# Optimization experiments

Measured on AMD Instinct MI355X. Metric: run time of the kernel, lower is better.

## Reference

```python
import jax, jax.numpy as jnp
import numpy as np

N_FREQ = 5
K = 16  # nneigh


def _gather(points, idx):
    # points: [B,N,C], idx: [B,nQ,K] -> [B,nQ,K,C]
    return jax.vmap(lambda p, i: p[i])(points, idx)


def setup_inputs() -> dict:
    key = jax.random.key(0)
    ks = jax.random.split(key, 16)
    B, nQ, N, dim_inp, dim = 2, 8192, 4096, 128, 128
    s = dim_inp ** -0.5
    return {
        "xyz_q": jax.random.uniform(ks[0], (B, nQ, 2), jnp.float32),
        "lat_rep": jax.random.normal(ks[1], (B, dim_inp), jnp.float32),
        "xyz": jax.random.uniform(ks[2], (B, N, 3), jnp.float32),
        "points": jax.random.normal(ks[3], (B, N, dim_inp), jnp.float32),
        "w_qs": jax.random.normal(ks[4], (dim_inp, dim), jnp.float32) * s,
        "w_ks": jax.random.normal(ks[5], (dim_inp, dim), jnp.float32) * s,
        "w_vs": jax.random.normal(ks[6], (dim_inp, dim), jnp.float32) * s,
        "w_kg": jax.random.normal(ks[7], (dim_inp, dim), jnp.float32) * s,
        "w_vg": jax.random.normal(ks[8], (dim_inp, dim), jnp.float32) * s,
        "gamma_w1": jax.random.normal(ks[9], (dim, dim), jnp.float32) * (dim ** -0.5),
        "gamma_b1": jnp.zeros((dim,), jnp.float32),
        "gamma_w2": jax.random.normal(ks[10], (dim, dim), jnp.float32) * (dim ** -0.5),
        "gamma_b2": jnp.zeros((dim,), jnp.float32),
        "pe_w": jax.random.normal(ks[11], (3 * 2 * N_FREQ + 3, dim), jnp.float32) * (33 ** -0.5),
        "pe_b": jnp.zeros((dim,), jnp.float32),
    }


def reference(xyz_q, lat_rep, xyz, points, w_qs, w_ks, w_vs, w_kg, w_vg,
              gamma_w1, gamma_b1, gamma_w2, gamma_b2, pe_w, pe_b):
    b, nQ, _ = xyz_q.shape
    dim = w_qs.shape[1]
    # kNN in 2D (no_grad in original): squared distance [B,nQ,N]
    dists = jnp.sum((xyz_q[:, :, None] - xyz[:, None, :, :2]) ** 2, axis=-1)
    _, knn_idx = jax.lax.top_k(-dists, K)  # ascending distance order

    # global latent [B,dim_inp] branch
    q_attn = (lat_rep @ w_qs)[:, None, None, :]          # [B,1,1,dim]
    k_global = jnp.broadcast_to((lat_rep @ w_kg)[:, None, None, :], (b, nQ, 1, dim))
    v_global = jnp.broadcast_to((lat_rep @ w_vg)[:, None, None, :], (b, nQ, 1, dim))

    k_attn = jnp.concatenate([_gather(points @ w_ks, knn_idx), k_global], axis=2)  # [B,nQ,K+1,dim]
    v_attn = jnp.concatenate([_gather(points @ w_vs, knn_idx), v_global], axis=2)

    xyz_knn = _gather(xyz, knn_idx)                      # [B,nQ,K,3]
    pos_diff = jnp.concatenate(
        [xyz_q[:, :, None] - xyz_knn[..., :2], xyz_knn[..., -1:]], axis=-1)  # [B,nQ,K,3]
    freq_bands = jnp.linspace(1.0, 2.0 ** N_FREQ, N_FREQ)
    embeds = [pos_diff]
    for fr in freq_bands:
        embeds.append(jnp.sin(pos_diff * fr))
        embeds.append(jnp.cos(pos_diff * fr))
    pos_embed = jnp.concatenate(embeds, axis=-1)         # [B,nQ,K,33]
    pos_encode = pos_embed @ pe_w + pe_b                 # [B,nQ,K,dim]
    pos_encode = jnp.concatenate(
        [pos_encode, jnp.zeros((b, nQ, 1, dim), pos_encode.dtype)], axis=2)  # [B,nQ,K+1,dim]

    h = q_attn - k_attn + pos_encode
    h = jnp.maximum(h @ gamma_w1 + gamma_b1, 0.0) @ gamma_w2 + gamma_b2
    attn = jax.nn.softmax(h, axis=-2)                    # softmax over neighbor axis
    res = jnp.sum(attn * (v_attn + pos_encode), axis=2)  # einsum 'bmnf,bmnf->bmf'
    return res
```

## Files before the change

### kernel.cpp

```cpp
#include <hip/hip_runtime.h>
#include <cstdint>

#define DIM   128
#define KNN   16
#define NB    2
#define NQ    8192
#define NPTS  4096
#define KVROWS 16
#define GRID  32
#define NCELL (GRID*GRID)
#define CAP   384

typedef unsigned short ushort_t;
typedef short vshort8 __attribute__((ext_vector_type(8)));
typedef float vfloat4 __attribute__((ext_vector_type(4)));

__device__ __forceinline__ ushort_t bf16_rne(float f) {
    unsigned u = __float_as_uint(f);
    unsigned r = u + 0x7FFFu + ((u >> 16) & 1u);
    return (ushort_t)(r >> 16);
}
__device__ __forceinline__ int cell_of(float x) {
    int c = (int)(x * 32.0f);
    return min(max(c, 0), GRID - 1);
}
__device__ __forceinline__ float f4_at(float4 v, int i) {
    return (i == 0) ? v.x : (i == 1) ? v.y : (i == 2) ? v.z : v.w;
}

__device__ __forceinline__ void pack_body(
    const float* __restrict__ src, int K, int ncols, int NT, int KS,
    ushort_t* __restrict__ dst, int gid)
{
    int total = NT*KS*64;
    if (gid >= total) return;
    int lane = gid & 63; int c = gid >> 6;
    int s = c % KS; int n = c / KS;
    int k0 = s*32 + ((lane >> 4) << 3);
    int col = n*16 + (lane & 15);
    vshort8 v;
    #pragma unroll
    for (int i = 0; i < 8; ++i) {
        int k = k0 + i;
        float f = (k < K) ? src[k*ncols + col] : 0.f;
        v[i] = (short)bf16_rne(f);
    }
    *(vshort8*)(dst + gid*8) = v;
}

__device__ __forceinline__ void scan1024(
    const int* __restrict__ cnt, int* __restrict__ cs, int* __restrict__ cu,
    int* __restrict__ ss, int t)
{
    int v0 = cnt[t*4 + 0];
    int v1 = cnt[t*4 + 1];
    int v2 = cnt[t*4 + 2];
    int v3 = cnt[t*4 + 3];
    int p0 = v0, p1 = p0 + v1, p2 = p1 + v2, p3 = p2 + v3;
    ss[t] = p3;
    __syncthreads();
    for (int off = 1; off < 256; off <<= 1) {
        int add = (t >= off) ? ss[t - off] : 0;
        __syncthreads();
        ss[t] += add;
        __syncthreads();
    }
    int excl = ss[t] - p3;
    cs[t*4 + 0] = excl;        cu[t*4 + 0] = excl;
    cs[t*4 + 1] = excl + p0;   cu[t*4 + 1] = excl + p0;
    cs[t*4 + 2] = excl + p1;   cu[t*4 + 2] = excl + p1;
    cs[t*4 + 3] = excl + p2;   cu[t*4 + 3] = excl + p2;
    if (t == 255) cs[NCELL] = ss[255];
}

__global__ __launch_bounds__(256) void pre1_k(
    const float* __restrict__ w_ks, const float* __restrict__ g_w1,
    const float* __restrict__ pe_w, const float* __restrict__ xyz,
    const float* __restrict__ xyz_q,
    float* __restrict__ Wk1, float* __restrict__ pwc,
    int* __restrict__ cellcnt, int* __restrict__ qcnt)
{
    int t = threadIdx.x; int bx = blockIdx.x;
    if (bx < 64) {
        int row = bx*2 + (t >> 7); int f = t & 127;
        float acc = 0.f;
        for (int c = 0; c < 128; ++c) acc = fmaf(w_ks[row*128 + c], g_w1[c*128 + f], acc);
        Wk1[row*128 + f] = acc;
    } else if (bx < 128) {
        int r = bx - 64; int col = t;
        float v = 0.f;
        if (r < 33) {
            if (col < 128) {
                float a = 0.f;
                for (int c = 0; c < 128; ++c) a = fmaf(pe_w[r*128 + c], g_w1[c*128 + col], a);
                v = a;
            } else {
                v = pe_w[r*128 + (col - 128)];
            }
        }
        pwc[r*256 + col] = v;
    } else if (bx < 160) {
        int gid = (bx - 128)*256 + t;
        int b = gid >> 12; int n = gid & (NPTS - 1);
        const float* p = xyz + (b*NPTS + n)*3;
        atomicAdd(&cellcnt[b*NCELL + cell_of(p[1])*GRID + cell_of(p[0])], 1);
    } else {
        int gid = (bx - 160)*256 + t;
        int b = gid >> 13; int q = gid & (NQ - 1);
        const float* p = xyz_q + (b*NQ + q)*2;
        atomicAdd(&qcnt[b*NCELL + cell_of(p[1])*GRID + cell_of(p[0])], 1);
    }
}

__global__ __launch_bounds__(256) void pre2_k(
    const float* __restrict__ pwc, const float* __restrict__ g_w2,
    const int* __restrict__ cnt, const int* __restrict__ qcnt,
    const float* __restrict__ lat, const float* __restrict__ w_qs,
    const float* __restrict__ w_kg, const float* __restrict__ w_vg,
    const float* __restrict__ g_w1, const float* __restrict__ g_b1,
    const float* __restrict__ pe_b,
    ushort_t* __restrict__ pwf, ushort_t* __restrict__ w2f,
    int* __restrict__ cell_start, int* __restrict__ cursor,
    int* __restrict__ qstart, int* __restrict__ qcursor,
    float* __restrict__ c1_out, float* __restrict__ vg_out, float* __restrict__ h2g_out)
{
    __shared__ int ss[256];
    __shared__ float qs[NB][DIM];
    __shared__ float hgx[NB][DIM];
    __shared__ float h1gx[NB][DIM];
    int t = threadIdx.x; int bx = blockIdx.x;
    if (bx < 4) {
        pack_body(pwc, 32, 256, 16, 1, pwf, bx*256 + t);
    } else if (bx < 12) {
        pack_body(g_w2, 128, 128, 8, 4, w2f, (bx - 4)*256 + t);
    } else if (bx < 14) {
        int b = bx - 12;
        scan1024(cnt + b*NCELL, cell_start + b*(NCELL+1), cursor + b*NCELL, ss, t);
    } else if (bx < 16) {
        int b = bx - 14;
        scan1024(qcnt + b*NCELL, qstart + b*(NCELL+1), qcursor + b*NCELL, ss, t);
    } else {
        int b = t >> 7; int f = t & 127;
        float aq = 0.f, ak = 0.f, av = 0.f;
        for (int c = 0; c < DIM; ++c) {
            float l = lat[b*DIM + c];
            aq = fmaf(l, w_qs[c*DIM + f], aq);
            ak = fmaf(l, w_kg[c*DIM + f], ak);
            av = fmaf(l, w_vg[c*DIM + f], av);
        }
        vg_out[b*DIM + f] = av;
        qs[b][f] = aq + pe_b[f];
        hgx[b][f] = aq - ak;
        __syncthreads();
        float acc = g_b1[f], acch = g_b1[f];
        for (int c = 0; c < DIM; ++c) {
            float w = g_w1[c*DIM + f];
            acc  = fmaf(qs[b][c], w, acc);
            acch = fmaf(hgx[b][c], w, acch);
        }
        c1_out[b*DIM + f] = acc;
        h1gx[b][f] = fmaxf(acch, 0.f);
        __syncthreads();
        float acc2 = 0.f;
        for (int c = 0; c < DIM; ++c) acc2 = fmaf(h1gx[b][c], g_w2[c*DIM + f], acc2);
        h2g_out[b*DIM + f] = acc2;
    }
}

__global__ __launch_bounds__(256) void pre3_k(
    const float* __restrict__ xyz, const float* __restrict__ xyz_q,
    int* __restrict__ cursor, int* __restrict__ qcursor,
    float2* __restrict__ sxy, int* __restrict__ sidx,
    float2* __restrict__ qsxy, int* __restrict__ qsidx)
{
    int t = threadIdx.x; int bx = blockIdx.x;
    if (bx < 32) {
        int gid = bx*256 + t;
        int b = gid >> 12; int n = gid & (NPTS - 1);
        const float* p = xyz + (b*NPTS + n)*3;
        float x = p[0], y = p[1];
        int slot = atomicAdd(&cursor[b*NCELL + cell_of(y)*GRID + cell_of(x)], 1);
        sxy[b*NPTS + slot] = make_float2(x, y);
        sidx[b*NPTS + slot] = n;
    } else {
        int gid = (bx - 32)*256 + t;
        int b = gid >> 13; int q = gid & (NQ - 1);
        const float* p = xyz_q + (b*NQ + q)*2;
        float x = p[0], y = p[1];
        int slot = atomicAdd(&qcursor[b*NCELL + cell_of(y)*GRID + cell_of(x)], 1);
        qsxy[b*NQ + slot] = make_float2(x, y);
        qsidx[b*NQ + slot] = q;
    }
}

__global__ __launch_bounds__(256) void knnkv_k(
    const float* __restrict__ points, const float* __restrict__ Wk1,
    const float* __restrict__ w_vs, const float* __restrict__ pe_b,
    const float* __restrict__ c1_,
    const float2* __restrict__ qsxy, const float2* __restrict__ sxy,
    const int* __restrict__ sidx, const int* __restrict__ cstart,
    float* __restrict__ K1c, float* __restrict__ Vp,
    int* __restrict__ knn_out)
{
    __shared__ __align__(16) float smem[4*CAP*2];
    int t = threadIdx.x; int bx = blockIdx.x;

    if (bx < 512) {
        float* pts = smem;
        int r0 = bx * KVROWS;
        int b = r0 >> 12;
        #pragma unroll
        for (int k = 0; k < KVROWS*DIM/256; ++k) {
            int e = t + k*256;
            pts[e] = points[r0*DIM + e];
        }
        __syncthreads();
        int f = t & 127; int mat = t >> 7;
        const float* W = mat ? w_vs : Wk1;
        float* O = mat ? Vp : K1c;
        float addv = mat ? pe_b[f] : c1_[b*DIM + f];
        float sgn  = mat ? 1.f : -1.f;
        int fc = (f & 15)*8 + (f >> 4);
        float acc[KVROWS];
        #pragma unroll
        for (int r = 0; r < KVROWS; ++r) acc[r] = 0.f;
        const float4* pts4 = reinterpret_cast<const float4*>(pts);
        for (int c4 = 0; c4 < DIM/4; ++c4) {
            float w0 = W[(c4*4+0)*DIM + f];
            float w1 = W[(c4*4+1)*DIM + f];
            float w2 = W[(c4*4+2)*DIM + f];
            float w3 = W[(c4*4+3)*DIM + f];
            #pragma unroll
            for (int r = 0; r < KVROWS; ++r) {
                float4 p = pts4[r*(DIM/4) + c4];
                acc[r] = fmaf(p.x, w0, acc[r]);
                acc[r] = fmaf(p.y, w1, acc[r]);
                acc[r] = fmaf(p.z, w2, acc[r]);
                acc[r] = fmaf(p.w, w3, acc[r]);
            }
        }
        #pragma unroll
        for (int r = 0; r < KVROWS; ++r) O[(r0 + r)*DIM + fc] = fmaf(sgn, acc[r], addv);
        return;
    }

    int bxk = bx - 512;
    int wid = t >> 6, lane = t & 63;
    int b = bxk >> 11; int q = (bxk & 2047)*4 + wid;
    float* cd = smem + wid*CAP;
    int*   ci = (int*)(smem + 4*CAP) + wid*CAP;
    float2 qp = qsxy[b*NQ + q];
    float xq = qp.x, yq = qp.y;
    int cx = cell_of(xq), cy = cell_of(yq);
    const int* cs_b = cstart + b*(NCELL+1);
    const float INF = 3.4e38f;
    const float CS = 1.0f/32.0f;
    int* outp = knn_out + (b*NQ + q)*KNN;
    unsigned long long lmask = (1ull << lane) - 1ull;

    for (int R = 2; R < 9; ++R) {
        int x0 = max(cx-R, 0), x1 = min(cx+R, GRID-1);
        int y0 = max(cy-R, 0), y1 = min(cy+R, GRID-1);
        int cnt = 0;
        for (int ry = y0; ry <= y1; ++ry) {
            int s0 = cs_b[ry*GRID + x0];
            int e0 = cs_b[ry*GRID + x1 + 1];
            for (int o = s0 + lane; o < e0; o += 64) {
                float2 p = sxy[b*NPTS + o];
                float dx = __fadd_rn(xq, -p.x);
                float dy = __fadd_rn(yq, -p.y);
                float d = __fadd_rn(__fmul_rn(dx, dx), __fmul_rn(dy, dy));
                int slot = cnt + (o - s0);
                if (slot < CAP) { cd[slot] = d; ci[slot] = o; }
            }
            cnt += e0 - s0;
        }
        asm volatile("s_waitcnt lgkmcnt(0)" ::: "memory");
        __builtin_amdgcn_sched_barrier(0);

        int cc = min(cnt, CAP);
        float dr[6];
        #pragma unroll
        for (int k = 0; k < 6; ++k)
            dr[k] = (lane + k*64 < cc) ? cd[lane + k*64] : INF;

        unsigned lo = 0u, hi = 0x40000000u;
        #pragma unroll 1
        for (int it = 0; it < 32; ++it) {
            if (hi - lo <= 1u) break;
            unsigned mid = (lo + hi) >> 1;
            float pv = __uint_as_float(mid);
            int c = 0;
            #pragma unroll
            for (int k = 0; k < 6; ++k)
                c += __popcll(__ballot(dr[k] <= pv));
            if (c >= KNN) {
                hi = mid;
                if (c == KNN) break;
            } else {
                lo = mid;
            }
        }
        float thr = __uint_as_float(hi);

        float bl = (x0 > 0)      ? (xq - (float)x0*CS)       : INF;
        float br = (x1 < GRID-1) ? ((float)(x1+1)*CS - xq)   : INF;
        float bb = (y0 > 0)      ? (yq - (float)y0*CS)       : INF;
        float bt = (y1 < GRID-1) ? ((float)(y1+1)*CS - yq)   : INF;
        float safe = fminf(fminf(bl, br), fminf(bb, bt)) - 2e-6f;
        bool whole = (safe > 1e8f);
        bool ok = (cnt >= KNN) && (cnt <= CAP) && (whole || thr <= safe*safe);
        if (ok || R == 8) {
            int base = 0;
            #pragma unroll
            for (int k = 0; k < 6; ++k) {
                bool p = dr[k] < thr;
                unsigned long long m = __ballot(p);
                int pos = base + __popcll(m & lmask);
                if (p && pos < KNN) outp[pos] = sidx[b*NPTS + ci[lane + k*64]];
                base += __popcll(m);
            }
            #pragma unroll
            for (int k = 0; k < 6; ++k) {
                bool p = dr[k] == thr;
                unsigned long long m = __ballot(p);
                int pos = base + __popcll(m & lmask);
                if (p && pos < KNN) outp[pos] = sidx[b*NPTS + ci[lane + k*64]];
                base += __popcll(m);
            }
            break;
        }
    }
}

__global__ __launch_bounds__(512, 2) void fuse_k(
    const float2* __restrict__ qsxy, const int* __restrict__ qsidx,
    const float* __restrict__ xyz,
    const float* __restrict__ K1c, const float* __restrict__ Vp,
    const int* __restrict__ knn_idx,
    const float* __restrict__ vg_, const float* __restrict__ h2g_,
    const float* __restrict__ pw32_,
    const ushort_t* __restrict__ pwf, const ushort_t* __restrict__ w2f,
    float* __restrict__ out)
{
    __shared__ __align__(16) ushort_t w2B[32*512];
    __shared__ __align__(16) ushort_t h1b[8][2048];

    int t = threadIdx.x, lane = t & 63, wid = t >> 6;
    int sid = (blockIdx.x & 7) * 64 + (blockIdx.x >> 3);
    int b = sid >> 8; int qbase = (sid & 255) * 32;

    {
        const int4* s2 = (const int4*)w2f;  int4* d2 = (int4*)w2B;
        #pragma unroll
        for (int i = 0; i < 4; ++i) d2[t + i*512] = s2[t + i*512];
    }
    __syncthreads();

    int c16 = lane & 15, g = lane >> 4, rowbase = g*4;
    ushort_t* hb = h1b[wid];
    const vshort8* pwBv = (const vshort8*)pwf;
    const vshort8* w2Bv = (const vshort8*)w2B;
    const float4* K4 = (const float4*)K1c;
    const float4* V4 = (const float4*)Vp;
    const vfloat4 vzero = (vfloat4){0.f, 0.f, 0.f, 0.f};

    float pw32r[16], hgr[8], vgr[8];
    #pragma unroll
    for (int n = 0; n < 16; ++n) pw32r[n] = pw32_[n*16 + c16];
    #pragma unroll
    for (int n = 0; n < 8; ++n) {
        hgr[n] = h2g_[b*128 + n*16 + c16];
        vgr[n] = vg_[b*128 + n*16 + c16];
    }

    #pragma unroll 1
    for (int qi = 0; qi < 4; ++qi) {
        int q = qbase + wid*4 + qi;
        float2 qp = qsxy[b*NQ + q];
        float xq = qp.x, yq = qp.y;
        int qorig = qsidx[b*NQ + q];
        int idxrow = knn_idx[(b*NQ + q)*KNN + c16];
        const float* p = xyz + (b*NPTS + idxrow)*3;
        float pd0 = xq - p[0], pd1 = yq - p[1], pd2 = p[2];
        int rf4[4];
        #pragma unroll
        for (int r = 0; r < 4; ++r)
            rf4[r] = (b*NPTS + __shfl(idxrow, rowbase + r))*32 + c16*2;

        vshort8 eh;
        int k0 = g*8;
        #pragma unroll
        for (int j = 0; j < 8; ++j) {
            int k = k0 + j;
            float v;
            if (k < 3) {
                v = (k == 0) ? pd0 : (k == 1 ? pd1 : pd2);
            } else {
                int m = k - 3; int fi = m / 6; int rem = m - fi*6;
                int comp = (rem < 3) ? rem : rem - 3;
                float pdc = (comp == 0) ? pd0 : (comp == 1 ? pd1 : pd2);
                float fr = (fi == 0) ? 1.0f : (fi == 1) ? 8.75f : (fi == 2) ? 16.5f
                         : (fi == 3) ? 24.25f : 32.0f;
                float arg = pdc * fr;
                v = (rem < 3) ? __sinf(arg) : __cosf(arg);
            }
            eh[j] = (short)bf16_rne(v);
        }
        float c32 = __cosf(32.0f * pd2);
        float c32r[4];
        #pragma unroll
        for (int r = 0; r < 4; ++r) c32r[r] = __shfl(c32, rowbase + r);

        #pragma unroll
        for (int half = 0; half < 2; ++half) {
            float4 k1q[4];
            #pragma unroll
            for (int r = 0; r < 4; ++r) k1q[r] = K4[rf4[r] + half];
            #pragma unroll
            for (int nn = 0; nn < 4; ++nn) {
                int n = half*4 + nn;
                vfloat4 a = __builtin_amdgcn_mfma_f32_16x16x32_bf16(
                    eh, pwBv[n*64 + lane], vzero, 0, 0, 0);
                int col = n*16 + c16;
                int s = col >> 5;
                int lp = ((col >> 3) & 3) << 4;
                int j = c16 & 7;
                #pragma unroll
                for (int r = 0; r < 4; ++r) {
                    float h = f4_at(k1q[r], nn) + fmaf(c32r[r], pw32r[n], a[r]);
                    h = fmaxf(h, 0.f);
                    hb[s*512 + (lp | (rowbase + r))*8 + j] = bf16_rne(h);
                }
            }
        }
        asm volatile("s_waitcnt lgkmcnt(0)" ::: "memory");
        __builtin_amdgcn_sched_barrier(0);

        vfloat4 acc2[8];
        #pragma unroll
        for (int n = 0; n < 8; ++n) acc2[n] = vzero;
        #pragma unroll
        for (int s = 0; s < 4; ++s) {
            vshort8 ah = ((const vshort8*)hb)[s*64 + lane];
            #pragma unroll
            for (int n = 0; n < 8; ++n) {
                vshort8 bh = w2Bv[(n*4 + s)*64 + lane];
                acc2[n] = __builtin_amdgcn_mfma_f32_16x16x32_bf16(ah, bh, acc2[n], 0, 0, 0);
            }
        }

        #pragma unroll
        for (int half = 0; half < 2; ++half) {
            float4 vq[4];
            #pragma unroll
            for (int r = 0; r < 4; ++r) vq[r] = V4[rf4[r] + half];
            #pragma unroll
            for (int nn = 0; nn < 4; ++nn) {
                int n = half*4 + nn;
                vfloat4 ap = __builtin_amdgcn_mfma_f32_16x16x32_bf16(
                    eh, pwBv[(8 + n)*64 + lane], vzero, 0, 0, 0);
                #pragma unroll
                for (int r = 0; r < 4; ++r) ap[r] = fmaf(c32r[r], pw32r[8 + n], ap[r]);

                float hg = hgr[n];
                vfloat4 a2 = acc2[n];
                float mx = fmaxf(fmaxf(a2[0], a2[1]), fmaxf(a2[2], a2[3]));
                mx = fmaxf(mx, __shfl_xor(mx, 16));
                mx = fmaxf(mx, __shfl_xor(mx, 32));
                mx = fmaxf(mx, hg);
                float sum = 0.f, num = 0.f;
                #pragma unroll
                for (int r = 0; r < 4; ++r) {
                    float ev = __expf(a2[r] - mx);
                    float v = f4_at(vq[r], nn) + ap[r];
                    sum += ev;
                    num = fmaf(ev, v, num);
                }
                sum += __shfl_xor(sum, 16); sum += __shfl_xor(sum, 32);
                num += __shfl_xor(num, 16); num += __shfl_xor(num, 32);
                float eg = __expf(hg - mx);
                sum += eg;
                num = fmaf(eg, vgr[n], num);
                if (g == 0) out[(b*NQ + qorig)*128 + n*16 + c16] = num / sum;
            }
        }
    }
}

extern "C" void kernel_launch(void* const* d_in, const int* in_sizes, int n_in,
                              void* d_out, int out_size, void* d_ws, size_t ws_size,
                              hipStream_t stream) {
    const float* xyz_q  = (const float*)d_in[0];
    const float* lat    = (const float*)d_in[1];
    const float* xyz    = (const float*)d_in[2];
    const float* points = (const float*)d_in[3];
    const float* w_qs   = (const float*)d_in[4];
    const float* w_ks   = (const float*)d_in[5];
    const float* w_vs   = (const float*)d_in[6];
    const float* w_kg   = (const float*)d_in[7];
    const float* w_vg   = (const float*)d_in[8];
    const float* g_w1   = (const float*)d_in[9];
    const float* g_b1   = (const float*)d_in[10];
    const float* g_w2   = (const float*)d_in[11];
    const float* g_b2   = (const float*)d_in[12];
    const float* pe_w   = (const float*)d_in[13];
    const float* pe_b   = (const float*)d_in[14];
    float* out = (float*)d_out;
    (void)g_b2;

    float* ws   = (float*)d_ws;
    float* Vp   = ws;
    float* K1c  = Vp  + NB*NPTS*DIM;
    float* Wk1  = K1c + NB*NPTS*DIM;
    float* pwc  = Wk1 + DIM*DIM;
    float* c1   = pwc + 64*256;
    float* vg   = c1  + NB*DIM;
    float* h2g  = vg  + NB*DIM;
    int*   knn  = (int*)(h2g + NB*DIM);
    ushort_t* pwf = (ushort_t*)(knn + NB*NQ*KNN);
    ushort_t* w2f = pwf + 16*64*8;
    int* cellcnt  = (int*)(w2f + 32*64*8);
    int* qcnt     = cellcnt + NB*NCELL;
    int* cellstart = qcnt + NB*NCELL;
    int* cursor    = cellstart + NB*(NCELL+1);
    int* qstart    = cursor + NB*NCELL;
    int* qcursor   = qstart + NB*(NCELL+1);
    int* sidx      = qcursor + NB*NCELL;
    float2* sxy    = (float2*)(sidx + NB*NPTS);
    int* qsidx     = (int*)(sxy + NB*NPTS);
    float2* qsxy   = (float2*)(qsidx + NB*NQ);

    hipMemsetAsync(cellcnt, 0, 2*NB*NCELL*sizeof(int), stream);
    pre1_k<<<224, 256, 0, stream>>>(w_ks, g_w1, pe_w, xyz, xyz_q,
                                    Wk1, pwc, cellcnt, qcnt);
    pre2_k<<<17, 256, 0, stream>>>(pwc, g_w2, cellcnt, qcnt,
                                   lat, w_qs, w_kg, w_vg, g_w1, g_b1, pe_b,
                                   pwf, w2f, cellstart, cursor, qstart, qcursor,
                                   c1, vg, h2g);
    pre3_k<<<96, 256, 0, stream>>>(xyz, xyz_q, cursor, qcursor,
                                   sxy, sidx, qsxy, qsidx);
    knnkv_k<<<512 + NB*NQ/4, 256, 0, stream>>>(points, Wk1, w_vs, pe_b, c1,
                                               qsxy, sxy, sidx, cellstart,
                                               K1c, Vp, knn);
    fuse_k<<<NB*NQ/32, 512, 0, stream>>>(qsxy, qsidx, xyz, K1c, Vp, knn, vg, h2g,
                                         pwc + 32*256, pwf, w2f, out);
}
```

Before: 111.9 us.

## Share kNN candidate gathering across four spatially sorted queries per wavefront

Result: no change. 113.5 us (+1.4%).

```diff
diff --git a/kernel.cpp b/kernel.cpp
--- a/kernel.cpp
+++ b/kernel.cpp
@@ -9,7 +9,7 @@
 #define KVROWS 16
 #define GRID  32
 #define NCELL (GRID*GRID)
-#define CAP   384
+#define CAP2  512
 
 typedef unsigned short ushort_t;
 typedef short vshort8 __attribute__((ext_vector_type(8)));
@@ -71,6 +71,88 @@
     cs[t*4 + 2] = excl + p1;   cu[t*4 + 2] = excl + p1;
     cs[t*4 + 3] = excl + p2;   cu[t*4 + 3] = excl + p2;
     if (t == 255) cs[NCELL] = ss[255];
+}
+
+__device__ __forceinline__ void knn_ring1(
+    float xq, float yq, int cgx, int cgy,
+    const float2* __restrict__ sxy_b, const int* __restrict__ sidx_b,
+    const int* __restrict__ cs_b,
+    float2* cxy, int* cidx, int lane, unsigned long long lmask,
+    int* __restrict__ outp)
+{
+    const float INF = 3.4e38f, CS = 1.0f/32.0f;
+    #pragma unroll 1
+    for (int R = 2; R < 9; ++R) {
+        int x0 = max(cgx - R, 0), x1 = min(cgx + R, GRID-1);
+        int y0 = max(cgy - R, 0), y1 = min(cgy + R, GRID-1);
+        int cnt = 0;
+        for (int ry = y0; ry <= y1; ++ry) {
+            int s0 = cs_b[ry*GRID + x0];
+            int e0 = cs_b[ry*GRID + x1 + 1];
+            for (int o = s0 + lane; o < e0; o += 64) {
+                int slot = cnt + (o - s0);
+                if (slot < CAP2) { cxy[slot] = sxy_b[o]; cidx[slot] = o; }
+            }
+            cnt += e0 - s0;
+        }
+        asm volatile("s_waitcnt lgkmcnt(0)" ::: "memory");
+        __builtin_amdgcn_sched_barrier(0);
+        int cc = min(cnt, CAP2);
+        int kact = (cc + 63) >> 6;
+        float dr[8];
+        #pragma unroll
+        for (int k = 0; k < 8; ++k) {
+            int id = lane + k*64;
+            if (id < cc) {
+                float2 p = cxy[id];
+                float dx = __fadd_rn(xq, -p.x);
+                float dy = __fadd_rn(yq, -p.y);
+                dr[k] = __fadd_rn(__fmul_rn(dx, dx), __fmul_rn(dy, dy));
+            } else dr[k] = INF;
+        }
+        unsigned lo = 0u, hi = 0x40000000u;
+        #pragma unroll 1
+        for (int it = 0; it < 32; ++it) {
+            if (hi - lo <= 1u) break;
+            unsigned mid = (lo + hi) >> 1;
+            float pv = __uint_as_float(mid);
+            int c = 0;
+            #pragma unroll
+            for (int k = 0; k < 8; ++k)
+                if (k < kact) c += __popcll(__ballot(dr[k] <= pv));
+            if (c >= KNN) { hi = mid; if (c == KNN) break; }
+            else lo = mid;
+        }
+        float thr = __uint_as_float(hi);
+        int base = 0;
+        #pragma unroll
+        for (int k = 0; k < 8; ++k) {
+            if (k < kact) {
+                bool pr = dr[k] < thr;
+                unsigned long long m = __ballot(pr);
+                int pos = base + __popcll(m & lmask);
+                if (pr && pos < KNN) outp[pos] = sidx_b[cidx[lane + k*64]];
+                base += __popcll(m);
+            }
+        }
+        #pragma unroll
+        for (int k = 0; k < 8; ++k) {
+            if (k < kact) {
+                bool pr = dr[k] == thr;
+                unsigned long long m = __ballot(pr);
+                int pos = base + __popcll(m & lmask);
+                if (pr && pos < KNN) outp[pos] = sidx_b[cidx[lane + k*64]];
+                base += __popcll(m);
+            }
+        }
+        float bl = (x0 > 0)      ? (xq - (float)x0*CS)     : INF;
+        float br = (x1 < GRID-1) ? ((float)(x1+1)*CS - xq) : INF;
+        float bb = (y0 > 0)      ? (yq - (float)y0*CS)     : INF;
+        float bt = (y1 < GRID-1) ? ((float)(y1+1)*CS - yq) : INF;
+        float safe = fminf(fminf(bl, br), fminf(bb, bt)) - 2e-6f;
+        bool whole = (x0 == 0 && y0 == 0 && x1 == GRID-1 && y1 == GRID-1);
+        if (cnt >= KNN && cnt <= CAP2 && (whole || thr <= safe*safe)) break;
+    }
 }
 
 __global__ __launch_bounds__(256) void pre1_k(
@@ -202,7 +284,7 @@
     float* __restrict__ K1c, float* __restrict__ Vp,
     int* __restrict__ knn_out)
 {
-    __shared__ __align__(16) float smem[4*CAP*2];
+    __shared__ __align__(16) float smem[6144];
     int t = threadIdx.x; int bx = blockIdx.x;
 
     if (bx < 512) {
@@ -246,89 +328,113 @@
 
     int bxk = bx - 512;
     int wid = t >> 6, lane = t & 63;
-    int b = bxk >> 11; int q = (bxk & 2047)*4 + wid;
-    float* cd = smem + wid*CAP;
-    int*   ci = (int*)(smem + 4*CAP) + wid*CAP;
-    float2 qp = qsxy[b*NQ + q];
-    float xq = qp.x, yq = qp.y;
-    int cx = cell_of(xq), cy = cell_of(yq);
+    int b = bxk >> 9; int qg = (bxk & 511)*16 + wid*4;
+    float2* cxy = (float2*)smem + wid*CAP2;
+    int*    cidx = (int*)(smem + 4096) + wid*CAP2;
+    const float2* sxy_b = sxy + b*NPTS;
+    const int* sidx_b = sidx + b*NPTS;
     const int* cs_b = cstart + b*(NCELL+1);
-    const float INF = 3.4e38f;
-    const float CS = 1.0f/32.0f;
-    int* outp = knn_out + (b*NQ + q)*KNN;
+    const float INF = 3.4e38f, CS = 1.0f/32.0f;
     unsigned long long lmask = (1ull << lane) - 1ull;
 
-    for (int R = 2; R < 9; ++R) {
-        int x0 = max(cx-R, 0), x1 = min(cx+R, GRID-1);
-        int y0 = max(cy-R, 0), y1 = min(cy+R, GRID-1);
-        int cnt = 0;
-        for (int ry = y0; ry <= y1; ++ry) {
-            int s0 = cs_b[ry*GRID + x0];
-            int e0 = cs_b[ry*GRID + x1 + 1];
-            for (int o = s0 + lane; o < e0; o += 64) {
-                float2 p = sxy[b*NPTS + o];
-                float dx = __fadd_rn(xq, -p.x);
-                float dy = __fadd_rn(yq, -p.y);
-                float d = __fadd_rn(__fmul_rn(dx, dx), __fmul_rn(dy, dy));
-                int slot = cnt + (o - s0);
-                if (slot < CAP) { cd[slot] = d; ci[slot] = o; }
-            }
-            cnt += e0 - s0;
-        }
-        asm volatile("s_waitcnt lgkmcnt(0)" ::: "memory");
-        __builtin_amdgcn_sched_barrier(0);
-
-        int cc = min(cnt, CAP);
-        float dr[6];
-        #pragma unroll
-        for (int k = 0; k < 6; ++k)
-            dr[k] = (lane + k*64 < cc) ? cd[lane + k*64] : INF;
-
-        unsigned lo = 0u, hi = 0x40000000u;
+    float xq[4], yq[4]; int cxi[4], cyi[4];
+    #pragma unroll
+    for (int i = 0; i < 4; ++i) {
+        float2 qp = qsxy[b*NQ + qg + i];
+        xq[i] = qp.x; yq[i] = qp.y;
+        cxi[i] = cell_of(qp.x); cyi[i] = cell_of(qp.y);
+    }
+    int x0g = min(min(cxi[0], cxi[1]), min(cxi[2], cxi[3]));
+    int x1g = max(max(cxi[0], cxi[1]), max(cxi[2], cxi[3]));
+    int y0g = min(min(cyi[0], cyi[1]), min(cyi[2], cyi[3]));
+    int y1g = max(max(cyi[0], cyi[1]), max(cyi[2], cyi[3]));
+
+    if (x1g - x0g <= 3 && y1g - y0g <= 3) {
         #pragma unroll 1
-        for (int it = 0; it < 32; ++it) {
-            if (hi - lo <= 1u) break;
-            unsigned mid = (lo + hi) >> 1;
-            float pv = __uint_as_float(mid);
-            int c = 0;
-            #pragma unroll
-            for (int k = 0; k < 6; ++k)
-                c += __popcll(__ballot(dr[k] <= pv));
-            if (c >= KNN) {
-                hi = mid;
-                if (c == KNN) break;
-            } else {
-                lo = mid;
-            }
-        }
-        float thr = __uint_as_float(hi);
-
-        float bl = (x0 > 0)      ? (xq - (float)x0*CS)       : INF;
-        float br = (x1 < GRID-1) ? ((float)(x1+1)*CS - xq)   : INF;
-        float bb = (y0 > 0)      ? (yq - (float)y0*CS)       : INF;
-        float bt = (y1 < GRID-1) ? ((float)(y1+1)*CS - yq)   : INF;
-        float safe = fminf(fminf(bl, br), fminf(bb, bt)) - 2e-6f;
-        bool whole = (safe > 1e8f);
-        bool ok = (cnt >= KNN) && (cnt <= CAP) && (whole || thr <= safe*safe);
-        if (ok || R == 8) {
-            int base = 0;
-            #pragma unroll
-            for (int k = 0; k < 6; ++k) {
-                bool p = dr[k] < thr;
-                unsigned long long m = __ballot(p);
-                int pos = base + __popcll(m & lmask);
-                if (p && pos < KNN) outp[pos] = sidx[b*NPTS + ci[lane + k*64]];
-                base += __popcll(m);
-            }
-            #pragma unroll
-            for (int k = 0; k < 6; ++k) {
-                bool p = dr[k] == thr;
-                unsigned long long m = __ballot(p);
-                int pos = base + __popcll(m & lmask);
-                if (p && pos < KNN) outp[pos] = sidx[b*NPTS + ci[lane + k*64]];
-                base += __popcll(m);
-            }
-            break;
+        for (int R = 2; R < 9; ++R) {
+            int x0 = max(x0g - R, 0), x1 = min(x1g + R, GRID-1);
+            int y0 = max(y0g - R, 0), y1 = min(y1g + R, GRID-1);
+            int cnt = 0;
+            for (int ry = y0; ry <= y1; ++ry) {
+                int s0 = cs_b[ry*GRID + x0];
+                int e0 = cs_b[ry*GRID + x1 + 1];
+                for (int o = s0 + lane; o < e0; o += 64) {
+                    int slot = cnt + (o - s0);
+                    if (slot < CAP2) { cxy[slot] = sxy_b[o]; cidx[slot] = o; }
+                }
+                cnt += e0 - s0;
+            }
+            asm volatile("s_waitcnt lgkmcnt(0)" ::: "memory");
+            __builtin_amdgcn_sched_barrier(0);
+
+            int cc = min(cnt, CAP2);
+            int kact = (cc + 63) >> 6;
+            bool whole = (x0 == 0 && y0 == 0 && x1 == GRID-1 && y1 == GRID-1);
+            bool okv[4];
+            #pragma unroll
+            for (int i = 0; i < 4; ++i) {
+                float dr[8];
+                #pragma unroll
+                for (int k = 0; k < 8; ++k) {
+                    int id = lane + k*64;
+                    if (id < cc) {
+                        float2 p = cxy[id];
+                        float dx = __fadd_rn(xq[i], -p.x);
+                        float dy = __fadd_rn(yq[i], -p.y);
+                        dr[k] = __fadd_rn(__fmul_rn(dx, dx), __fmul_rn(dy, dy));
+                    } else dr[k] = INF;
+                }
+                unsigned lo = 0u, hi = 0x40000000u;
+                #pragma unroll 1
+                for (int it = 0; it < 32; ++it) {
+                    if (hi - lo <= 1u) break;
+                    unsigned mid = (lo + hi) >> 1;
+                    float pv = __uint_as_float(mid);
+                    int c = 0;
+                    #pragma unroll
+                    for (int k = 0; k < 8; ++k)
+                        if (k < kact) c += __popcll(__ballot(dr[k] <= pv));
+                    if (c >= KNN) { hi = mid; if (c == KNN) break; }
+                    else lo = mid;
+                }
+                float thr = __uint_as_float(hi);
+                int* outp = knn_out + (b*NQ + qg + i)*KNN;
+                int base = 0;
+                #pragma unroll
+                for (int k = 0; k < 8; ++k) {
+                    if (k < kact) {
+                        bool pr = dr[k] < thr;
+                        unsigned long long m = __ballot(pr);
+                        int pos = base + __popcll(m & lmask);
+                        if (pr && pos < KNN) outp[pos] = sidx_b[cidx[lane + k*64]];
+                        base += __popcll(m);
+                    }
+                }
+                #pragma unroll
+                for (int k = 0; k < 8; ++k) {
+                    if (k < kact) {
+                        bool pr = dr[k] == thr;
+                        unsigned long long m = __ballot(pr);
+                        int pos = base + __popcll(m & lmask);
+                        if (pr && pos < KNN) outp[pos] = sidx_b[cidx[lane + k*64]];
+                        base += __popcll(m);
+                    }
+                }
+                float bl = (x0 > 0)      ? (xq[i] - (float)x0*CS)     : INF;
+                float br = (x1 < GRID-1) ? ((float)(x1+1)*CS - xq[i]) : INF;
+                float bb = (y0 > 0)      ? (yq[i] - (float)y0*CS)     : INF;
+                float bt = (y1 < GRID-1) ? ((float)(y1+1)*CS - yq[i]) : INF;
+                float safe = fminf(fminf(bl, br), fminf(bb, bt)) - 2e-6f;
+                okv[i] = (cnt >= KNN) && (cnt <= CAP2) && (whole || thr <= safe*safe);
+            }
+            if ((okv[0] && okv[1] && okv[2] && okv[3]) || R == 8) break;
+        }
+    } else {
+        #pragma unroll
+        for (int i = 0; i < 4; ++i) {
+            knn_ring1(xq[i], yq[i], cxi[i], cyi[i], sxy_b, sidx_b, cs_b,
+                      cxy, cidx, lane, lmask,
+                      knn_out + (b*NQ + qg + i)*KNN);
         }
     }
 }
@@ -540,9 +646,9 @@
                                    c1, vg, h2g);
     pre3_k<<<96, 256, 0, stream>>>(xyz, xyz_q, cursor, qcursor,
                                    sxy, sidx, qsxy, qsidx);
-    knnkv_k<<<512 + NB*NQ/4, 256, 0, stream>>>(points, Wk1, w_vs, pe_b, c1,
-                                               qsxy, sxy, sidx, cellstart,
-                                               K1c, Vp, knn);
+    knnkv_k<<<512 + NB*NQ/16, 256, 0, stream>>>(points, Wk1, w_vs, pe_b, c1,
+                                                qsxy, sxy, sidx, cellstart,
+                                                K1c, Vp, knn);
     fuse_k<<<NB*NQ/32, 512, 0, stream>>>(qsxy, qsidx, xyz, K1c, Vp, knn, vg, h2g,
                                          pwc + 32*256, pwf, w2f, out);
 }
```
